# Optimization experiments

Hardware: AMD Instinct MI355X
Metric: run time of the kernel (lower is better)

Reference implementation:

```python
import jax, jax.numpy as jnp
import numpy as np

H = 8  # heads, hard-coded in the original module


def setup_inputs() -> dict:
    key = jax.random.key(0)
    ks = jax.random.split(key, 7)
    B, Lq, Lkv = 4, 2048, 512
    dim_q, dim_kv = 1024, 768
    q = jax.random.normal(ks[0], (B, Lq, dim_q), dtype=jnp.float32)
    kv = jax.random.normal(ks[1], (B, Lkv, dim_kv), dtype=jnp.float32)
    # Linear weights stored as [in, out] so y = x @ W (math-equivalent to torch Linear)
    Wq = jax.random.normal(ks[2], (dim_q, dim_q), dtype=jnp.float32) / np.sqrt(dim_q)
    Wk = jax.random.normal(ks[3], (dim_kv, dim_q), dtype=jnp.float32) / np.sqrt(dim_kv)
    Wv = jax.random.normal(ks[4], (dim_kv, dim_q), dtype=jnp.float32) / np.sqrt(dim_kv)
    Wo = jax.random.normal(ks[5], (dim_q, dim_q), dtype=jnp.float32) / np.sqrt(dim_q)
    bo = jax.random.normal(ks[6], (dim_q,), dtype=jnp.float32) * 0.01
    return {"q": q, "kv": kv, "Wq": Wq, "Wk": Wk, "Wv": Wv, "Wo": Wo, "bo": bo}


def reference(q, kv, Wq, Wk, Wv, Wo, bo):
    B, Lq, dim_q = q.shape
    hd = dim_q // H
    scale = jnp.asarray(hd, q.dtype) ** -0.5
    # projections
    qp = q @ Wq   # [B, Lq, dim_q]
    kp = kv @ Wk  # [B, Lkv, dim_q]
    vp = kv @ Wv  # [B, Lkv, dim_q]
    # split heads: [B, L, H, hd]
    qh = qp.reshape(B, Lq, H, hd)
    kh = kp.reshape(B, kv.shape[1], H, hd)
    vh = vp.reshape(B, kv.shape[1], H, hd)
    # scaled attention scores and softmax
    scores = jnp.einsum("bqhd,bkhd->bhqk", qh, kh) * scale
    attn = jax.nn.softmax(scores, axis=-1)
    out = jnp.einsum("bhqk,bkhd->bqhd", attn, vh).reshape(B, Lq, dim_q)
    return out @ Wo + bo
```

## Files before the change

kernel.cpp:

```cpp
#include <hip/hip_runtime.h>
#include <hip/hip_cooperative_groups.h>

namespace cg = cooperative_groups;


typedef unsigned short u16;
typedef unsigned int u32;
using short8  = __attribute__((ext_vector_type(8))) short;
using floatx4 = __attribute__((ext_vector_type(4))) float;

__device__ inline u16 f2bf(float x) {
  union { float f; u32 u; } v; v.f = x;
  u32 r = (v.u + 0x7fffu + ((v.u >> 16) & 1u)) >> 16;
  return (u16)r;
}

__device__ inline float fast_exp2(float x) {
#if __has_builtin(__builtin_amdgcn_exp2f)
  return __builtin_amdgcn_exp2f(x);
#else
  return exp2f(x);
#endif
}

#define MFMA(a, b, c) __builtin_amdgcn_mfma_f32_16x16x32_bf16(a, b, c, 0, 0, 0)

__device__ inline void async_lds16(const void* g, void* l) {
  __builtin_amdgcn_global_load_lds(
      (const __attribute__((address_space(1))) void*)g,
      (__attribute__((address_space(3))) void*)l, 16, 0, 0);
}

#define WAIT_VM(n) { asm volatile("s_waitcnt vmcnt(" #n ")" ::: "memory"); \
                     __builtin_amdgcn_sched_barrier(0); }
#define WAIT_LGKM0 { asm volatile("s_waitcnt lgkmcnt(0)" ::: "memory"); \
                     __builtin_amdgcn_sched_barrier(0); }
#define SBAR       { __builtin_amdgcn_s_barrier(); \
                     __builtin_amdgcn_sched_barrier(0); }

__device__ __forceinline__
void cvt_body(const float* __restrict__ q, const float* __restrict__ kv,
              u16* __restrict__ q_bf, u16* __restrict__ kv_bf, int lin) {
  for (int i = lin * 256 + (int)threadIdx.x; i < 1245184; i += 262144) {
    const float* src; u16* dst; int idx;
    if (i < 1048576) { src = q;  dst = q_bf;  idx = i; }
    else             { src = kv; dst = kv_bf; idx = i - 1048576; }
    float4 a = ((const float4*)src)[2 * idx];
    float4 b = ((const float4*)src)[2 * idx + 1];
    u16 t[8] = {f2bf(a.x), f2bf(a.y), f2bf(a.z), f2bf(a.w),
                f2bf(b.x), f2bf(b.y), f2bf(b.z), f2bf(b.w)};
    ((short8*)dst)[idx] = *(short8*)t;
  }
}

__device__ __forceinline__
void transpose_body(int bid, const float* __restrict__ Wq, const float* __restrict__ Wk,
                    const float* __restrict__ Wv, const float* __restrict__ Wo,
                    u16* __restrict__ WqT, u16* __restrict__ WkvT, u16* __restrict__ WoT,
                    float* __restrict__ tile ) {
  const int z = bid >> 8;
  const float* W; u16* Wt; int K;
  if      (z == 0) { W = Wq; Wt = WqT;               K = 1024; }
  else if (z == 1) { W = Wk; Wt = WkvT;              K = 768;  }
  else if (z == 2) { W = Wv; Wt = WkvT + 1024 * 768; K = 768;  }
  else             { W = Wo; Wt = WoT;               K = 1024; }
  const int k0 = ((bid >> 4) & 15) * 64, n0 = (bid & 15) * 64;
  if (k0 >= K) return;
  const int N = 1024;
  const int t = threadIdx.x;
  for (int p = 0; p < 4; ++p) {
    int cid = p * 256 + t;
    int row = cid >> 4, c = cid & 15;
    float4 v = *(const float4*)&W[(long)(k0 + row) * N + n0 + c * 4];
    tile[row * 68 + c * 4 + 0] = v.x; tile[row * 68 + c * 4 + 1] = v.y;
    tile[row * 68 + c * 4 + 2] = v.z; tile[row * 68 + c * 4 + 3] = v.w;
  }
  __syncthreads();
  for (int p = 0; p < 2; ++p) {
    int oc = p * 256 + t;
    int n = oc >> 3, c = oc & 7;
    u16 tmp[8];
    for (int s = 0; s < 8; ++s) tmp[s] = f2bf(tile[(c * 8 + s) * 68 + n]);
    *(short8*)&Wt[(long)(n0 + n) * K + k0 + c * 8] = *(short8*)tmp;
  }
}

__device__ __forceinline__
void gemm_body(const u16* __restrict__ A, const u16* __restrict__ Bt,
               u16* __restrict__ Cb, float* __restrict__ Cf,
               const float* __restrict__ bias, u16* __restrict__ vt_out,
               int K, int ldc, int lin, int mt_per_xcd, u16* smem) {
  const int tid  = threadIdx.x;
  const int wave = tid >> 6, lane = tid & 63;
  const int l15  = lane & 15, quad = lane >> 4;
  const int wm   = (wave >> 1) * 64, wn = (wave & 1) * 64;
  const int xcd  = lin & 7, slot = lin >> 3;
  const int mt   = xcd * mt_per_xcd + (slot % mt_per_xcd);
  const int nti  = slot / mt_per_xcd;
  const long m0  = (long)mt * 128, n0 = (long)nti * 128;

  const int pl  = lane >> 3;
  const int gg  = (lane & 7) ^ pl;
  const int ro  = pl * 2 + (gg >> 2);
  const int co  = (gg & 3) * 8;
  const u16* Aw = A  + (m0 + wave * 32 + ro) * (long)K + co;
  const u16* Bw = Bt + (n0 + wave * 32 + ro) * (long)K + co;
  u16* const A0 = smem;        u16* const B0 = smem + 4096;
  u16* const A1 = smem + 8192; u16* const B1 = smem + 12288;
  const int rdo  = ((((l15 & 1) << 2) | quad) ^ (l15 >> 1)) * 8;
  const int aoff = wm * 32 + (l15 >> 1) * 64 + rdo;
  const int boff = wn * 32 + (l15 >> 1) * 64 + rdo;

#define STAGE_G(Ab, Bb, kk)                                          \
  { async_lds16(Aw + (kk),                (Ab) + wave * 1024);       \
    async_lds16(Aw + 16 * (long)K + (kk), (Ab) + wave * 1024 + 512); \
    async_lds16(Bw + (kk),                (Bb) + wave * 1024);       \
    async_lds16(Bw + 16 * (long)K + (kk), (Bb) + wave * 1024 + 512); }

  floatx4 acc[4][4] = {};
  STAGE_G(A0, B0, 0);
  const int NS = K >> 5;
  for (int s = 0; s < NS; ++s) {
    u16* Ac = (s & 1) ? A1 : A0; u16* Bc = (s & 1) ? B1 : B0;
    if (s + 1 < NS) {
      u16* An = (s & 1) ? A0 : A1; u16* Bn = (s & 1) ? B0 : B1;
      STAGE_G(An, Bn, (s + 1) * 32);
      WAIT_VM(4);
    } else {
      WAIT_VM(0);
    }
    SBAR;
    short8 af[4], bfr[4];
    for (int i = 0; i < 4; ++i) af[i]  = *(const short8*)&Ac[aoff + i * 512];
    for (int j = 0; j < 4; ++j) bfr[j] = *(const short8*)&Bc[boff + j * 512];
    for (int i = 0; i < 4; ++i)
      for (int j = 0; j < 4; ++j)
        acc[i][j] = MFMA(af[i], bfr[j], acc[i][j]);
    WAIT_LGKM0;
    SBAR;
  }
#undef STAGE_G

  if (Cf) {
    for (int i = 0; i < 4; ++i)
      for (int j = 0; j < 4; ++j) {
        long row = m0 + wm + i * 16 + quad * 4;
        long col = n0 + wn + j * 16 + l15;
        float b = bias ? bias[col] : 0.f;
        for (int r = 0; r < 4; ++r) Cf[(row + r) * (long)ldc + col] = acc[i][j][r] + b;
      }
    return;
  }
  for (int i = 0; i < 4; ++i)
    for (int j = 0; j < 4; ++j)
      for (int r = 0; r < 4; ++r)
        smem[(wm + i * 16 + quad * 4 + r) * 138 + wn + j * 16 + l15] = f2bf(acc[i][j][r]);
  __syncthreads();
  if (vt_out && nti >= 8) {
    const int h  = nti - 8;
    const int bq = (int)(m0 >> 9);
    const int l0 = (int)(m0 & 511);
    u16* vbase = vt_out + ((long)(bq * 8 + h) * 128) * 512;
    for (int p = 0; p < 8; ++p) {
      int cid = p * 256 + tid;
      int d = cid >> 4, c = cid & 15;
      u16 tmp[8];
      for (int s = 0; s < 8; ++s) tmp[s] = smem[(c * 8 + s) * 138 + d];
      *(short8*)&vbase[(long)d * 512 + l0 + c * 8] = *(short8*)tmp;
    }
  } else {
    for (int p = 0; p < 8; ++p) {
      int cid = p * 256 + tid;
      int row = cid >> 4, c = cid & 15;
      short8 v = *(const short8*)&smem[row * 138 + c * 8];
      *(short8*)&Cb[(m0 + row) * (long)ldc + n0 + c * 8] = v;
    }
  }
}

__device__ __forceinline__
void attn_body(const u16* __restrict__ qp, const u16* __restrict__ kp,
               const u16* __restrict__ vT, u16* __restrict__ ctx,
               int lin, u16* smem) {
  u16* Ks = smem;
  u16* Vs = smem + 8192;
  const int tid  = threadIdx.x;
  const int wave = tid >> 6, lane = tid & 63;
  u16* Pw = smem + 16384 + wave * 1024;
  const int l15  = lane & 15, quad = lane >> 4;
  const int xcd  = lin & 7, slot = lin >> 3;
  const int pairIdx = xcd * 4 + (slot & 3);
  const int b = pairIdx >> 3, h = pairIdx & 7;
  const int qtile = slot >> 2;
  const long rowbase = (long)b * 2048 + qtile * 64 + wave * 16;
  const float sc = 0.08838834764831845f * 1.4426950408889634f;

  short8 aQ[4];
  for (int dc = 0; dc < 4; ++dc)
    aQ[dc] = *(const short8*)&qp[(rowbase + l15) * 1024 + h * 128 + dc * 32 + quad * 8];

  floatx4 O[8] = {};
  float lsum[4] = {};
  const u16* kpb   = kp + ((long)b * 512) * 1024 + h * 128;
  const u16* vbase = vT + ((long)(b * 8 + h) * 128) * 512;

  const int krow = lane >> 4;
  const int kpos = lane & 15;
  const int vrow = lane >> 3;
  const int vpos = lane & 7;

#define STAGE_K(t)                                                             \
  for (int i = 0; i < 4; ++i) {                                                \
    int inst = wave * 4 + i;                                                   \
    int row  = inst * 4 + krow;                                                \
    int g    = kpos ^ (row & 15);                                              \
    async_lds16(kpb + (long)((t) * 64 + row) * 1024 + g * 8, &Ks[inst * 512]); \
  }
#define STAGE_V(t)                                                             \
  for (int i = 0; i < 4; ++i) {                                                \
    int inst = wave * 4 + i;                                                   \
    int d    = inst * 8 + vrow;                                                \
    int g    = vpos ^ (d & 7);                                                 \
    async_lds16(vbase + (long)d * 512 + (t) * 64 + g * 8, &Vs[inst * 512]);    \
  }

  STAGE_K(0);
  STAGE_V(0);
  for (int t = 0; t < 8; ++t) {
    WAIT_VM(4);
    SBAR;
    floatx4 S[4] = {};
    __builtin_amdgcn_s_setprio(1);
    for (int dc = 0; dc < 4; ++dc)
      for (int ks = 0; ks < 4; ++ks) {
        int k = ks * 16 + l15;
        short8 bk = *(const short8*)&Ks[k * 128 + (((dc * 4 + quad) ^ l15) * 8)];
        S[ks] = MFMA(aQ[dc], bk, S[ks]);
      }
    __builtin_amdgcn_s_setprio(0);
    WAIT_LGKM0;
    SBAR;
    if (t < 7) STAGE_K(t + 1);
    for (int ks = 0; ks < 4; ++ks)
      for (int r = 0; r < 4; ++r) {
        float p = fast_exp2(S[ks][r] * sc);
        lsum[r] += p;
        int row = quad * 4 + r;
        int g   = (ks * 2 + (l15 >> 3)) ^ (row & 7);
        Pw[row * 64 + g * 8 + (l15 & 7)] = f2bf(p);
      }
    short8 aP[2];
    for (int kc = 0; kc < 2; ++kc)
      aP[kc] = *(const short8*)&Pw[l15 * 64 + (((kc * 4 + quad) ^ (l15 & 7)) * 8)];
    if (t < 7) { WAIT_VM(4); }
    else       { WAIT_VM(0); }
    SBAR;
    __builtin_amdgcn_s_setprio(1);
    for (int j = 0; j < 8; ++j) {
      int d = j * 16 + l15;
      short8 bV0 = *(const short8*)&Vs[d * 64 + ((quad ^ (l15 & 7)) * 8)];
      short8 bV1 = *(const short8*)&Vs[d * 64 + (((4 + quad) ^ (l15 & 7)) * 8)];
      O[j] = MFMA(aP[0], bV0, O[j]);
      O[j] = MFMA(aP[1], bV1, O[j]);
    }
    __builtin_amdgcn_s_setprio(0);
    WAIT_LGKM0;
    SBAR;
    if (t < 7) STAGE_V(t + 1);
  }
#undef STAGE_K
#undef STAGE_V

  for (int r = 0; r < 4; ++r) {
    float sum = lsum[r];
    for (int off = 1; off < 16; off <<= 1) sum += __shfl_xor(sum, off);
    lsum[r] = 1.f / sum;
  }
  for (int j = 0; j < 8; ++j)
    for (int r = 0; r < 4; ++r)
      ctx[(rowbase + quad * 4 + r) * 1024 + h * 128 + j * 16 + l15] =
          f2bf(O[j][r] * lsum[r]);
}

__global__ __launch_bounds__(256, 4)
void mega(const float* q, const float* kv, const float* Wq, const float* Wk,
          const float* Wv, const float* Wo,
          u16* q_bf, u16* kv_bf, u16* WqT, u16* WkvT, u16* WoT,
          u16* qp, u16* kp, u16* vT, u16* ctx, float* out, const float* bo) {
  __shared__ __align__(16) u16 smem[20480];
  cg::grid_group g = cg::this_grid();
  const int bid = blockIdx.x;

  cvt_body(q, kv, q_bf, kv_bf, bid);
  transpose_body(bid, Wq, Wk, Wv, Wo, WqT, WkvT, WoT, (float*)smem);
  g.sync();

  if (bid < 768) {
    const bool isQ = bid < 512;
    gemm_body(isQ ? q_bf : kv_bf, isQ ? WqT : WkvT, isQ ? qp : kp,
              nullptr, nullptr, isQ ? (u16*)nullptr : vT,
              isQ ? 1024 : 768, 1024, isQ ? bid : bid - 512, isQ ? 8 : 2, smem);
  }
  g.sync();
  attn_body(qp, kp, vT, ctx, bid, smem);
  g.sync();
  if (bid < 512)
    gemm_body(ctx, WoT, nullptr, out, bo, nullptr, 1024, 1024, bid, 8, smem);
}

__global__ void cvt_all(const float* __restrict__ q, const float* __restrict__ kv,
                        u16* __restrict__ q_bf, u16* __restrict__ kv_bf) {
  int i = blockIdx.x * 256 + threadIdx.x;
  const float* src; u16* dst; int idx;
  if (i < 1048576) { src = q;  dst = q_bf;  idx = i; }
  else             { src = kv; dst = kv_bf; idx = i - 1048576; }
  float4 a = ((const float4*)src)[2 * idx];
  float4 b = ((const float4*)src)[2 * idx + 1];
  u16 t[8] = {f2bf(a.x), f2bf(a.y), f2bf(a.z), f2bf(a.w),
              f2bf(b.x), f2bf(b.y), f2bf(b.z), f2bf(b.w)};
  ((short8*)dst)[idx] = *(short8*)t;
}
__global__ __launch_bounds__(256)
void transpose_all(const float* __restrict__ Wq, const float* __restrict__ Wk,
                   const float* __restrict__ Wv, const float* __restrict__ Wo,
                   u16* __restrict__ WqT, u16* __restrict__ WkvT, u16* __restrict__ WoT) {
  __shared__ __align__(16) float tile[64 * 68];
  int bid = blockIdx.x + blockIdx.y * 16 + blockIdx.z * 256;
  transpose_body(bid, Wq, Wk, Wv, Wo, WqT, WkvT, WoT, tile);
}
__global__ __launch_bounds__(256)
void k_proj_q(const u16* __restrict__ q_bf, const u16* __restrict__ WqT,
              u16* __restrict__ qp) {
  __shared__ __align__(16) u16 smem[17664];
  gemm_body(q_bf, WqT, qp, nullptr, nullptr, nullptr, 1024, 1024, blockIdx.x, 8, smem);
}
__global__ __launch_bounds__(256)
void k_proj_kv(const u16* __restrict__ kv_bf, const u16* __restrict__ WkvT,
               u16* __restrict__ kp, u16* __restrict__ vT) {
  __shared__ __align__(16) u16 smem[17664];
  gemm_body(kv_bf, WkvT, kp, nullptr, nullptr, vT, 768, 1024, blockIdx.x, 2, smem);
}
__global__ __launch_bounds__(256, 4)
void k_attn(const u16* __restrict__ qp, const u16* __restrict__ kp,
            const u16* __restrict__ vT, u16* __restrict__ ctx) {
  __shared__ __align__(16) u16 smem[20480];
  attn_body(qp, kp, vT, ctx, blockIdx.x, smem);
}
__global__ __launch_bounds__(256)
void k_oproj(const u16* __restrict__ ctx, const u16* __restrict__ WoT,
             float* __restrict__ out, const float* __restrict__ bo) {
  __shared__ __align__(16) u16 smem[17664];
  gemm_body(ctx, WoT, nullptr, out, bo, nullptr, 1024, 1024, blockIdx.x, 8, smem);
}

extern "C" void kernel_launch(void* const* d_in, const int* in_sizes, int n_in,
                              void* d_out, int out_size, void* d_ws, size_t ws_size,
                              hipStream_t stream) {
  const float* q  = (const float*)d_in[0];
  const float* kv = (const float*)d_in[1];
  const float* Wq = (const float*)d_in[2];
  const float* Wk = (const float*)d_in[3];
  const float* Wv = (const float*)d_in[4];
  const float* Wo = (const float*)d_in[5];
  const float* bo = (const float*)d_in[6];
  float* out = (float*)d_out;

  char* ws = (char*)d_ws;
  u16* q_bf  = (u16*)(ws + 0);
  u16* kv_bf = (u16*)(ws + 16777216);
  u16* WqT   = (u16*)(ws + 19922944);
  u16* WkvT  = (u16*)(ws + 22020096);
  u16* WoT   = (u16*)(ws + 25165824);
  u16* qp    = (u16*)(ws + 27262976);
  u16* kp    = (u16*)(ws + 44040192);
  u16* vT    = (u16*)(ws + 52428800);
  u16* ctx   = (u16*)(ws + 56623104);

  int maxb = 0;
  hipError_t oe = hipOccupancyMaxActiveBlocksPerMultiprocessor(
      &maxb, (const void*)mega, 256, 0);
  if (oe == hipSuccess && maxb >= 4) {
    void* args[] = {(void*)&q,    (void*)&kv,    (void*)&Wq,   (void*)&Wk,
                    (void*)&Wv,   (void*)&Wo,    (void*)&q_bf, (void*)&kv_bf,
                    (void*)&WqT,  (void*)&WkvT,  (void*)&WoT,  (void*)&qp,
                    (void*)&kp,   (void*)&vT,    (void*)&ctx,  (void*)&out,
                    (void*)&bo};
    hipLaunchCooperativeKernel((const void*)mega, dim3(1024), dim3(256),
                               args, 0, stream);
  } else {
    cvt_all<<<4864, 256, 0, stream>>>(q, kv, q_bf, kv_bf);
    transpose_all<<<dim3(16, 16, 4), 256, 0, stream>>>(Wq, Wk, Wv, Wo, WqT, WkvT, WoT);
    k_proj_q<<<512, 256, 0, stream>>>(q_bf, WqT, qp);
    k_proj_kv<<<256, 256, 0, stream>>>(kv_bf, WkvT, kp, vT);
    k_attn<<<1024, 256, 0, stream>>>(qp, kp, vT, ctx);
    k_oproj<<<512, 256, 0, stream>>>(ctx, WoT, out, bo);
  }
}
```

Baseline: 199.1 us.

## Replace cooperative megakernel with four fused launches and 512-thread attention blocks

Drops the cooperative megakernel and its grid-wide syncs in favour of four ordinary launches: a combined convert/transpose prep kernel, a merged Q/KV projection kernel, the attention kernel and the output projection. The attention kernel now runs 512-thread blocks covering 128 query rows, so each K/V tile staged in LDS is shared by twice as many waves and each wave issues half the async loads. This removes grid-barrier cost and the occupancy limits the cooperative launch imposed, at the price of extra launch gaps between stages and larger LDS use per attention block.

```diff
diff --git a/kernel.cpp b/kernel.cpp
--- a/kernel.cpp
+++ b/kernel.cpp
@@ -1,7 +1,4 @@
 #include <hip/hip_runtime.h>
-#include <hip/hip_cooperative_groups.h>
-
-namespace cg = cooperative_groups;
 
 
 typedef unsigned short u16;
@@ -37,21 +34,6 @@
                      __builtin_amdgcn_sched_barrier(0); }
 #define SBAR       { __builtin_amdgcn_s_barrier(); \
                      __builtin_amdgcn_sched_barrier(0); }
-
-__device__ __forceinline__
-void cvt_body(const float* __restrict__ q, const float* __restrict__ kv,
-              u16* __restrict__ q_bf, u16* __restrict__ kv_bf, int lin) {
-  for (int i = lin * 256 + (int)threadIdx.x; i < 1245184; i += 262144) {
-    const float* src; u16* dst; int idx;
-    if (i < 1048576) { src = q;  dst = q_bf;  idx = i; }
-    else             { src = kv; dst = kv_bf; idx = i - 1048576; }
-    float4 a = ((const float4*)src)[2 * idx];
-    float4 b = ((const float4*)src)[2 * idx + 1];
-    u16 t[8] = {f2bf(a.x), f2bf(a.y), f2bf(a.z), f2bf(a.w),
-                f2bf(b.x), f2bf(b.y), f2bf(b.z), f2bf(b.w)};
-    ((short8*)dst)[idx] = *(short8*)t;
-  }
-}
 
 __device__ __forceinline__
 void transpose_body(int bid, const float* __restrict__ Wq, const float* __restrict__ Wk,
@@ -82,6 +64,29 @@
     u16 tmp[8];
     for (int s = 0; s < 8; ++s) tmp[s] = f2bf(tile[(c * 8 + s) * 68 + n]);
     *(short8*)&Wt[(long)(n0 + n) * K + k0 + c * 8] = *(short8*)tmp;
+  }
+}
+
+__global__ __launch_bounds__(256)
+void k_prep(const float* __restrict__ q, const float* __restrict__ kv,
+            u16* __restrict__ q_bf, u16* __restrict__ kv_bf,
+            const float* __restrict__ Wq, const float* __restrict__ Wk,
+            const float* __restrict__ Wv, const float* __restrict__ Wo,
+            u16* __restrict__ WqT, u16* __restrict__ WkvT, u16* __restrict__ WoT) {
+  __shared__ __align__(16) float tile[64 * 68];
+  const int bid = blockIdx.x;
+  if (bid < 4864) {
+    int i = bid * 256 + threadIdx.x;
+    const float* src; u16* dst; int idx;
+    if (i < 1048576) { src = q;  dst = q_bf;  idx = i; }
+    else             { src = kv; dst = kv_bf; idx = i - 1048576; }
+    float4 a = ((const float4*)src)[2 * idx];
+    float4 b = ((const float4*)src)[2 * idx + 1];
+    u16 t[8] = {f2bf(a.x), f2bf(a.y), f2bf(a.z), f2bf(a.w),
+                f2bf(b.x), f2bf(b.y), f2bf(b.z), f2bf(b.w)};
+    ((short8*)dst)[idx] = *(short8*)t;
+  } else {
+    transpose_body(bid - 4864, Wq, Wk, Wv, Wo, WqT, WkvT, WoT, tile);
   }
 }
 
@@ -178,12 +183,25 @@
   }
 }
 
-__device__ __forceinline__
-void attn_body(const u16* __restrict__ qp, const u16* __restrict__ kp,
-               const u16* __restrict__ vT, u16* __restrict__ ctx,
-               int lin, u16* smem) {
+__global__ __launch_bounds__(256)
+void k_proj_qkv(const u16* __restrict__ q_bf, const u16* __restrict__ WqT,
+                const u16* __restrict__ kv_bf, const u16* __restrict__ WkvT,
+                u16* __restrict__ qp, u16* __restrict__ kp, u16* __restrict__ vT) {
+  __shared__ __align__(16) u16 smem[17664];
+  const int bid = blockIdx.x;
+  if (bid < 512)
+    gemm_body(q_bf, WqT, qp, nullptr, nullptr, nullptr, 1024, 1024, bid, 8, smem);
+  else
+    gemm_body(kv_bf, WkvT, kp, nullptr, nullptr, vT, 768, 1024, bid - 512, 2, smem);
+}
+
+__global__ __launch_bounds__(512)
+void k_attn(const u16* __restrict__ qp, const u16* __restrict__ kp,
+            const u16* __restrict__ vT, u16* __restrict__ ctx) {
+  __shared__ __align__(16) u16 smem[24576];
   u16* Ks = smem;
   u16* Vs = smem + 8192;
+  const int lin  = blockIdx.x;
   const int tid  = threadIdx.x;
   const int wave = tid >> 6, lane = tid & 63;
   u16* Pw = smem + 16384 + wave * 1024;
@@ -192,7 +210,7 @@
   const int pairIdx = xcd * 4 + (slot & 3);
   const int b = pairIdx >> 3, h = pairIdx & 7;
   const int qtile = slot >> 2;
-  const long rowbase = (long)b * 2048 + qtile * 64 + wave * 16;
+  const long rowbase = (long)b * 2048 + qtile * 128 + wave * 16;
   const float sc = 0.08838834764831845f * 1.4426950408889634f;
 
   short8 aQ[4];
@@ -210,15 +228,15 @@
   const int vpos = lane & 7;
 
 #define STAGE_K(t)                                                             \
-  for (int i = 0; i < 4; ++i) {                                                \
-    int inst = wave * 4 + i;                                                   \
+  for (int i = 0; i < 2; ++i) {                                                \
+    int inst = wave * 2 + i;                                                   \
     int row  = inst * 4 + krow;                                                \
     int g    = kpos ^ (row & 15);                                              \
     async_lds16(kpb + (long)((t) * 64 + row) * 1024 + g * 8, &Ks[inst * 512]); \
   }
 #define STAGE_V(t)                                                             \
-  for (int i = 0; i < 4; ++i) {                                                \
-    int inst = wave * 4 + i;                                                   \
+  for (int i = 0; i < 2; ++i) {                                                \
+    int inst = wave * 2 + i;                                                   \
     int d    = inst * 8 + vrow;                                                \
     int g    = vpos ^ (d & 7);                                                 \
     async_lds16(vbase + (long)d * 512 + (t) * 64 + g * 8, &Vs[inst * 512]);    \
@@ -227,7 +245,7 @@
   STAGE_K(0);
   STAGE_V(0);
   for (int t = 0; t < 8; ++t) {
-    WAIT_VM(4);
+    WAIT_VM(2);
     SBAR;
     floatx4 S[4] = {};
     __builtin_amdgcn_s_setprio(1);
@@ -252,7 +270,7 @@
     short8 aP[2];
     for (int kc = 0; kc < 2; ++kc)
       aP[kc] = *(const short8*)&Pw[l15 * 64 + (((kc * 4 + quad) ^ (l15 & 7)) * 8)];
-    if (t < 7) { WAIT_VM(4); }
+    if (t < 7) { WAIT_VM(2); }
     else       { WAIT_VM(0); }
     SBAR;
     __builtin_amdgcn_s_setprio(1);
@@ -282,70 +300,6 @@
           f2bf(O[j][r] * lsum[r]);
 }
 
-__global__ __launch_bounds__(256, 4)
-void mega(const float* q, const float* kv, const float* Wq, const float* Wk,
-          const float* Wv, const float* Wo,
-          u16* q_bf, u16* kv_bf, u16* WqT, u16* WkvT, u16* WoT,
-          u16* qp, u16* kp, u16* vT, u16* ctx, float* out, const float* bo) {
-  __shared__ __align__(16) u16 smem[20480];
-  cg::grid_group g = cg::this_grid();
-  const int bid = blockIdx.x;
-
-  cvt_body(q, kv, q_bf, kv_bf, bid);
-  transpose_body(bid, Wq, Wk, Wv, Wo, WqT, WkvT, WoT, (float*)smem);
-  g.sync();
-
-  if (bid < 768) {
-    const bool isQ = bid < 512;
-    gemm_body(isQ ? q_bf : kv_bf, isQ ? WqT : WkvT, isQ ? qp : kp,
-              nullptr, nullptr, isQ ? (u16*)nullptr : vT,
-              isQ ? 1024 : 768, 1024, isQ ? bid : bid - 512, isQ ? 8 : 2, smem);
-  }
-  g.sync();
-  attn_body(qp, kp, vT, ctx, bid, smem);
-  g.sync();
-  if (bid < 512)
-    gemm_body(ctx, WoT, nullptr, out, bo, nullptr, 1024, 1024, bid, 8, smem);
-}
-
-__global__ void cvt_all(const float* __restrict__ q, const float* __restrict__ kv,
-                        u16* __restrict__ q_bf, u16* __restrict__ kv_bf) {
-  int i = blockIdx.x * 256 + threadIdx.x;
-  const float* src; u16* dst; int idx;
-  if (i < 1048576) { src = q;  dst = q_bf;  idx = i; }
-  else             { src = kv; dst = kv_bf; idx = i - 1048576; }
-  float4 a = ((const float4*)src)[2 * idx];
-  float4 b = ((const float4*)src)[2 * idx + 1];
-  u16 t[8] = {f2bf(a.x), f2bf(a.y), f2bf(a.z), f2bf(a.w),
-              f2bf(b.x), f2bf(b.y), f2bf(b.z), f2bf(b.w)};
-  ((short8*)dst)[idx] = *(short8*)t;
-}
-__global__ __launch_bounds__(256)
-void transpose_all(const float* __restrict__ Wq, const float* __restrict__ Wk,
-                   const float* __restrict__ Wv, const float* __restrict__ Wo,
-                   u16* __restrict__ WqT, u16* __restrict__ WkvT, u16* __restrict__ WoT) {
-  __shared__ __align__(16) float tile[64 * 68];
-  int bid = blockIdx.x + blockIdx.y * 16 + blockIdx.z * 256;
-  transpose_body(bid, Wq, Wk, Wv, Wo, WqT, WkvT, WoT, tile);
-}
-__global__ __launch_bounds__(256)
-void k_proj_q(const u16* __restrict__ q_bf, const u16* __restrict__ WqT,
-              u16* __restrict__ qp) {
-  __shared__ __align__(16) u16 smem[17664];
-  gemm_body(q_bf, WqT, qp, nullptr, nullptr, nullptr, 1024, 1024, blockIdx.x, 8, smem);
-}
-__global__ __launch_bounds__(256)
-void k_proj_kv(const u16* __restrict__ kv_bf, const u16* __restrict__ WkvT,
-               u16* __restrict__ kp, u16* __restrict__ vT) {
-  __shared__ __align__(16) u16 smem[17664];
-  gemm_body(kv_bf, WkvT, kp, nullptr, nullptr, vT, 768, 1024, blockIdx.x, 2, smem);
-}
-__global__ __launch_bounds__(256, 4)
-void k_attn(const u16* __restrict__ qp, const u16* __restrict__ kp,
-            const u16* __restrict__ vT, u16* __restrict__ ctx) {
-  __shared__ __align__(16) u16 smem[20480];
-  attn_body(qp, kp, vT, ctx, blockIdx.x, smem);
-}
 __global__ __launch_bounds__(256)
 void k_oproj(const u16* __restrict__ ctx, const u16* __restrict__ WoT,
              float* __restrict__ out, const float* __restrict__ bo) {
@@ -376,23 +330,9 @@
   u16* vT    = (u16*)(ws + 52428800);
   u16* ctx   = (u16*)(ws + 56623104);
 
-  int maxb = 0;
-  hipError_t oe = hipOccupancyMaxActiveBlocksPerMultiprocessor(
-      &maxb, (const void*)mega, 256, 0);
-  if (oe == hipSuccess && maxb >= 4) {
-    void* args[] = {(void*)&q,    (void*)&kv,    (void*)&Wq,   (void*)&Wk,
-                    (void*)&Wv,   (void*)&Wo,    (void*)&q_bf, (void*)&kv_bf,
-                    (void*)&WqT,  (void*)&WkvT,  (void*)&WoT,  (void*)&qp,
-                    (void*)&kp,   (void*)&vT,    (void*)&ctx,  (void*)&out,
-                    (void*)&bo};
-    hipLaunchCooperativeKernel((const void*)mega, dim3(1024), dim3(256),
-                               args, 0, stream);
-  } else {
-    cvt_all<<<4864, 256, 0, stream>>>(q, kv, q_bf, kv_bf);
-    transpose_all<<<dim3(16, 16, 4), 256, 0, stream>>>(Wq, Wk, Wv, Wo, WqT, WkvT, WoT);
-    k_proj_q<<<512, 256, 0, stream>>>(q_bf, WqT, qp);
-    k_proj_kv<<<256, 256, 0, stream>>>(kv_bf, WkvT, kp, vT);
-    k_attn<<<1024, 256, 0, stream>>>(qp, kp, vT, ctx);
-    k_oproj<<<512, 256, 0, stream>>>(ctx, WoT, out, bo);
-  }
-}
+  k_prep<<<5888, 256, 0, stream>>>(q, kv, q_bf, kv_bf, Wq, Wk, Wv, Wo,
+                                   WqT, WkvT, WoT);
+  k_proj_qkv<<<768, 256, 0, stream>>>(q_bf, WqT, kv_bf, WkvT, qp, kp, vT);
+  k_attn<<<512, 512, 0, stream>>>(qp, kp, vT, ctx);
+  k_oproj<<<512, 256, 0, stream>>>(ctx, WoT, out, bo);
+}
```

Result: faster. 183.0 us (-8.1%).
